# Kernel tuning notes

Hardware: AMD Instinct MI355X
Metric: run time of the kernel (lower is better)

Reference implementation:

```python
import jax, jax.numpy as jnp
import numpy as np

LAYERS = 2
HEADS = 4
TYPE_IDX = 1  # type='logic' -> 1
HIDDEN = 256
HEAD_DIM = HIDDEN // HEADS
EPS = 1e-6


def setup_inputs() -> dict:
    key = jax.random.key(0)
    ks = jax.random.split(key, 12)
    B, S, H = 4, 2048, HIDDEN
    inputs = jax.random.normal(ks[0], (B, S, H), jnp.float32)
    graphs = jax.random.uniform(ks[1], (B, 2, S, S), jnp.float32)
    biases_batch = jax.random.normal(ks[2], (B, 2, S, S), jnp.float32)
    s_h = 1.0 / np.sqrt(H).astype(np.float32)
    s_d = 1.0 / np.sqrt(HEAD_DIM).astype(np.float32)
    gc_w = jax.random.normal(ks[3], (LAYERS, H, H), jnp.float32) * s_h
    gc_b = jnp.zeros((LAYERS, H), jnp.float32)
    attn_w = jax.random.normal(ks[4], (LAYERS, HEAD_DIM, H), jnp.float32) * s_h  # conv1 (1x1) weight
    attn_a = jax.random.normal(ks[5], (LAYERS, HEAD_DIM), jnp.float32) * s_d     # conv2_1 (1x1) weight
    ln_a = jnp.ones((H,), jnp.float32)
    ln_b = jnp.zeros((H,), jnp.float32)
    w1 = jax.random.normal(ks[6], (H, H), jnp.float32) * s_h
    w1b = jnp.zeros((H,), jnp.float32)
    w2 = jax.random.normal(ks[7], (H, H), jnp.float32) * s_h
    w2b = jnp.zeros((H,), jnp.float32)
    return dict(inputs=inputs, graphs=graphs, biases_batch=biases_batch,
                gc_w=gc_w, gc_b=gc_b, attn_w=attn_w, attn_a=attn_a,
                ln_a=ln_a, ln_b=ln_b, w1=w1, w1b=w1b, w2=w2, w2b=w2b)


def reference(inputs, graphs, biases_batch, gc_w, gc_b, attn_w, attn_a, ln_a, ln_b, w1, w1b, w2, w2b):
    adj = graphs[:, TYPE_IDX]          # [b,s,s]
    bias = biases_batch[:, TYPE_IDX]   # [b,s,s]
    x0 = inputs
    x = inputs
    for i in range(LAYERS):
        # GraphConvolution: adj @ (x @ W) + b
        mf = jnp.einsum('bij,bjh->bih', adj, x @ gc_w[i]) + gc_b[i]
        # Node_Attn_head (NOTE: original uses conv2_1 for BOTH f_1 and f_2)
        seq_fts = jnp.einsum('bsh,dh->bsd', mf, attn_w[i])      # [b,s,d]
        f = seq_fts @ attn_a[i]                                  # [b,s]
        logits = jax.nn.leaky_relu(f[:, :, None] + f[:, None, :])  # f_2^T + f_1 -> [b,s,s]
        coefs = jax.nn.softmax(logits + bias, axis=1)            # Softmax(dim=1)
        ret = jax.nn.leaky_relu(jnp.einsum('bij,bjd->bid', coefs, seq_fts))  # [b,s,d]
        # shared attention head across all HEADS -> identical outputs, concatenated
        x = jnp.tile(ret, (1, 1, HEADS)) + x
    # LayerNorm (torch.std is unbiased -> ddof=1), residual to original inputs
    mean = x.mean(-1, keepdims=True)
    std = jnp.std(x, axis=-1, keepdims=True, ddof=1)
    g = ln_a * (x - mean) / (std + EPS) + ln_b + x0
    # PositionwiseFeedForward (dropout inactive in eval)
    ff = jax.nn.relu(g @ w1.T + w1b) @ w2.T + w2b
    return ff + g
```

## Files before the change

### kernel.cpp

```cpp
#include <hip/hip_runtime.h>
#include <math.h>

#define BB 4
#define SS 2048
#define HH 256
#define DD 64
#define NLAYERS 2
#define NPART 128

#define XSC  (1.f/64.f)
#define XSCI 64.f
#define FSC  (1.f/256.f)
#define WSC  256.f
#define LNWSC 5.5451774444795624f
#define EC1  190781.31f
#define CWC  1.3418535e-3f

typedef _Float16 f16;
typedef f16 half8 __attribute__((ext_vector_type(8)));
typedef f16 half4 __attribute__((ext_vector_type(4)));
typedef float f32x4 __attribute__((ext_vector_type(4)));
#define MFMA16(a, b, c) __builtin_amdgcn_mfma_f32_16x16x32_f16(a, b, c, 0, 0, 0)

__device__ __forceinline__ float lrelu(float v) { return v > 0.f ? v : 0.01f * v; }
__device__ __forceinline__ int enc(float f) { int i = __float_as_int(f); return i >= 0 ? i : (i ^ 0x7fffffff); }
__device__ __forceinline__ float dec(int k) { int i = k >= 0 ? k : (k ^ 0x7fffffff); return __int_as_float(i); }
__device__ __forceinline__ void split8(const float* v, half8& h, half8& l) {
    #pragma unroll
    for (int e = 0; e < 8; ++e) {
        f16 hh = (f16)v[e]; h[e] = hh; l[e] = (f16)((v[e] - (float)hh) * 2048.f);
    }
}

__global__ __launch_bounds__(256) void prep_all(
    const float* __restrict__ gc_w, const float* __restrict__ gc_b,
    const float* __restrict__ attn_w,
    f16* __restrict__ WysH, f16* __restrict__ WysL, float* __restrict__ by,
    const float* __restrict__ w1, const float* __restrict__ w2,
    f16* __restrict__ w1h, f16* __restrict__ w1l,
    f16* __restrict__ w2h, f16* __restrict__ w2l, int* __restrict__ FMXi,
    const float* __restrict__ inputs, f16* __restrict__ xh, f16* __restrict__ xl)
{
    if (blockIdx.x >= 128) {
        long i = ((long)(blockIdx.x - 128) * 256 + threadIdx.x) * 8;
        float4 a = *(const float4*)&inputs[i];
        float4 b = *(const float4*)&inputs[i + 4];
        float v[8] = {a.x * XSC, a.y * XSC, a.z * XSC, a.w * XSC,
                      b.x * XSC, b.y * XSC, b.z * XSC, b.w * XSC};
        half8 h, l; split8(v, h, l);
        *(half8*)&xh[i] = h; *(half8*)&xl[i] = l;
        return;
    }
    int L = blockIdx.x >> 6, d = blockIdx.x & 63;
    int h = threadIdx.x;
    const float* gwr = gc_w + (long)L * HH * HH + (long)h * HH;
    const float* aw = attn_w + (long)L * DD * HH + (long)d * HH;
    float acc = 0.f;
    #pragma unroll 4
    for (int hp = 0; hp < HH; hp += 4) {
        float4 g4 = *(const float4*)&gwr[hp];
        float4 a4 = *(const float4*)&aw[hp];
        acc += g4.x * a4.x + g4.y * a4.y + g4.z * a4.z + g4.w * a4.w;
    }
    f16 hh = (f16)acc;
    WysH[((long)L * DD + d) * HH + h] = hh;
    WysL[((long)L * DD + d) * HH + h] = (f16)((acc - (float)hh) * 2048.f);
    if (h == 0) {
        float ba = 0.f;
        const float* gb = gc_b + (long)L * HH;
        for (int hp = 0; hp < HH; ++hp) ba += gb[hp] * aw[hp];
        by[L * DD + d] = ba;
    }
    int gt = blockIdx.x * 256 + h;
    #pragma unroll
    for (int p = 0; p < 4; ++p) {
        int e = gt * 4 + p;
        if (e < 65536) {
            float v = w1[e]; f16 x = (f16)v;
            w1h[e] = x; w1l[e] = (f16)((v - (float)x) * 2048.f);
        } else {
            int e2 = e - 65536;
            float v = w2[e2]; f16 x = (f16)v;
            w2h[e2] = x; w2l[e2] = (f16)((v - (float)x) * 2048.f);
        }
    }
    if (blockIdx.x == 0 && h < 2 * BB) FMXi[h] = enc(-1e30f);
}

__global__ __launch_bounds__(256) void y_mfma(
    const f16* __restrict__ xh, const f16* __restrict__ xl,
    const f16* __restrict__ WyhL, const f16* __restrict__ WylL,
    f16* __restrict__ yTh, f16* __restrict__ yTl)
{
    const int tid = threadIdx.x;
    const int w = tid >> 6, l = tid & 63;
    const int gw = blockIdx.x * 4 + w;
    const int b = gw >> 7, st = gw & 127;
    const int s0 = st * 16;
    const int lr = l & 15, kg = (l >> 4) * 8;
    const f16* Aph = xh + ((long)b * SS + s0 + lr) * HH;
    const f16* Apl = xl + ((long)b * SS + s0 + lr) * HH;
    f32x4 acch[4] = {}, accm[4] = {};
    #pragma unroll
    for (int k0 = 0; k0 < HH; k0 += 32) {
        half8 ah = *(const half8*)(Aph + k0 + kg);
        half8 al = *(const half8*)(Apl + k0 + kg);
        #pragma unroll
        for (int dt = 0; dt < 4; ++dt) {
            long boff = (long)(dt * 16 + lr) * HH + k0 + kg;
            half8 bh = *(const half8*)(WyhL + boff);
            half8 bl = *(const half8*)(WylL + boff);
            acch[dt] = MFMA16(ah, bh, acch[dt]);
            accm[dt] = MFMA16(ah, bl, accm[dt]);
            accm[dt] = MFMA16(al, bh, accm[dt]);
        }
    }
    const int rg0 = (l >> 4) * 4;
    #pragma unroll
    for (int dt = 0; dt < 4; ++dt) {
        int d = dt * 16 + lr;
        half4 h4, l4;
        #pragma unroll
        for (int rr = 0; rr < 4; ++rr) {
            float v = acch[dt][rr] + accm[dt][rr] * (1.f / 2048.f);
            f16 hh = (f16)v; h4[rr] = hh; l4[rr] = (f16)((v - (float)hh) * 2048.f);
        }
        long ob = ((long)b * DD + d) * SS + s0 + rg0;
        *(half4*)(yTh + ob) = h4;
        *(half4*)(yTl + ob) = l4;
    }
}

__global__ __launch_bounds__(512, 2) void ftp_fused(
    const float* __restrict__ adjB,
    const f16* __restrict__ yTh, const f16* __restrict__ yTl,
    const float* __restrict__ byL, const float* __restrict__ aaL,
    float* __restrict__ F, f16* __restrict__ fTh, f16* __restrict__ fTl,
    int* __restrict__ fmxSlot)
{
    __shared__ float Ls[8][16][68];
    __shared__ float fmaxS[16];
    const int b = blockIdx.y;
    const int i0 = blockIdx.x * 16;
    const int tid = threadIdx.x;
    const int w = tid >> 6, l = tid & 63, lr = l & 15, kg = (l >> 4) * 8;
    const float* Arow = adjB + (long)b * 2 * SS * SS + (long)(i0 + lr) * SS;
    const f16* Bh = yTh + ((long)b * DD + lr) * SS;
    const f16* Bl = yTl + ((long)b * DD + lr) * SS;

    f32x4 acch[4] = {}, accm[4] = {};
    #pragma unroll
    for (int ks = 0; ks < 256; ks += 32) {
        int k = w * 256 + ks + kg;
        float4 a0 = *(const float4*)(Arow + k);
        float4 a1 = *(const float4*)(Arow + k + 4);
        float av[8] = {a0.x, a0.y, a0.z, a0.w, a1.x, a1.y, a1.z, a1.w};
        half8 ah, al; split8(av, ah, al);
        #pragma unroll
        for (int dt = 0; dt < 4; ++dt) {
            long off = (long)dt * 16 * SS + k;
            half8 bh = *(const half8*)(Bh + off);
            half8 bl = *(const half8*)(Bl + off);
            acch[dt] = MFMA16(ah, bh, acch[dt]);
            accm[dt] = MFMA16(ah, bl, accm[dt]);
            accm[dt] = MFMA16(al, bh, accm[dt]);
        }
    }
    const int rg0 = (l >> 4) * 4;
    #pragma unroll
    for (int dt = 0; dt < 4; ++dt)
        #pragma unroll
        for (int rr = 0; rr < 4; ++rr)
            Ls[w][rg0 + rr][dt * 16 + lr] = acch[dt][rr] + accm[dt][rr] * (1.f / 2048.f);
    __syncthreads();

    {
        int r = tid >> 5, q = tid & 31, c0 = q * 2;
        float s0 = 0.f, s1 = 0.f;
        #pragma unroll
        for (int ww = 0; ww < 8; ++ww) { s0 += Ls[ww][r][c0]; s1 += Ls[ww][r][c0 + 1]; }
        s0 = s0 * XSCI + byL[c0];
        s1 = s1 * XSCI + byL[c0 + 1];
        Ls[0][r][c0] = s0; Ls[0][r][c0 + 1] = s1;
        float dot = s0 * aaL[c0] + s1 * aaL[c0 + 1];
        dot += __shfl_xor(dot, 1, 64);
        dot += __shfl_xor(dot, 2, 64);
        dot += __shfl_xor(dot, 4, 64);
        dot += __shfl_xor(dot, 8, 64);
        dot += __shfl_xor(dot, 16, 64);
        if (q == 0) { F[b * SS + i0 + r] = dot; fmaxS[r] = dot; }
    }
    __syncthreads();
    if (tid == 0) {
        float m = -1e30f;
        #pragma unroll
        for (int r = 0; r < 16; ++r) m = fmaxf(m, fmaxS[r]);
        atomicMax(fmxSlot + b, enc(m));
    }
    if (tid < 256) {
        int d = tid >> 2, sq = (tid & 3) * 4;
        half4 h4, l4;
        #pragma unroll
        for (int e = 0; e < 4; ++e) {
            float v = Ls[0][sq + e][d] * FSC;
            f16 hh = (f16)v; h4[e] = hh; l4[e] = (f16)((v - (float)hh) * 2048.f);
        }
        long ob = ((long)b * DD + d) * SS + i0 + sq;
        *(half4*)(fTh + ob) = h4;
        *(half4*)(fTl + ob) = l4;
    }
}

__global__ __launch_bounds__(512) void col_stats_part(
    const float* __restrict__ biasb, const float* __restrict__ f,
    const int* __restrict__ fmxSlot,
    float* __restrict__ partS, float* __restrict__ Mv, f16* __restrict__ EhL)
{
    __shared__ float fs[32];
    const int b = blockIdx.z;
    const int chunk = blockIdx.y;
    const int half = threadIdx.x >> 8;
    const int t = threadIdx.x & 255;
    const int j0 = blockIdx.x * 1024 + t * 4;
    const float* bb = biasb + (long)b * 2 * SS * SS;
    const int ibase = chunk * 32 + half * 16;

    if (threadIdx.x < 32) fs[threadIdx.x] = f[b * SS + chunk * 32 + threadIdx.x];

    float fj[4], M[4], s[4] = {0.f, 0.f, 0.f, 0.f};
    const float fmx = dec(fmxSlot[b]);
    #pragma unroll
    for (int q = 0; q < 4; ++q) {
        fj[q] = f[b * SS + j0 + q];
        M[q] = lrelu(fmx + fj[q]) + 8.f;
    }
    __syncthreads();

    #pragma unroll
    for (int ii = 0; ii < 16; ii += 2) {
        float fi0 = fs[half * 16 + ii], fi1 = fs[half * 16 + ii + 1];
        float4 b0 = *(const float4*)&bb[(long)(ibase + ii) * SS + j0];
        float4 b1 = *(const float4*)&bb[(long)(ibase + ii + 1) * SS + j0];
        float e00 = __expf(lrelu(fi0 + fj[0]) + b0.x - M[0]);
        float e01 = __expf(lrelu(fi0 + fj[1]) + b0.y - M[1]);
        float e02 = __expf(lrelu(fi0 + fj[2]) + b0.z - M[2]);
        float e03 = __expf(lrelu(fi0 + fj[3]) + b0.w - M[3]);
        float e10 = __expf(lrelu(fi1 + fj[0]) + b1.x - M[0]);
        float e11 = __expf(lrelu(fi1 + fj[1]) + b1.y - M[1]);
        float e12 = __expf(lrelu(fi1 + fj[2]) + b1.z - M[2]);
        float e13 = __expf(lrelu(fi1 + fj[3]) + b1.w - M[3]);
        s[0] += e00 + e10; s[1] += e01 + e11;
        s[2] += e02 + e12; s[3] += e03 + e13;
        if (EhL) {
            half4 h0, h1;
            h0[0] = (f16)(e00 * EC1); h0[1] = (f16)(e01 * EC1);
            h0[2] = (f16)(e02 * EC1); h0[3] = (f16)(e03 * EC1);
            h1[0] = (f16)(e10 * EC1); h1[1] = (f16)(e11 * EC1);
            h1[2] = (f16)(e12 * EC1); h1[3] = (f16)(e13 * EC1);
            *(half4*)&EhL[((long)b * SS + ibase + ii) * SS + j0] = h0;
            *(half4*)&EhL[((long)b * SS + ibase + ii + 1) * SS + j0] = h1;
        }
    }
    const int c = chunk * 2 + half;
    #pragma unroll
    for (int q = 0; q < 4; ++q)
        partS[((long)c * BB + b) * SS + j0 + q] = s[q];
    if (c == 0) {
        #pragma unroll
        for (int q = 0; q < 4; ++q) Mv[b * SS + j0 + q] = M[q];
    }
}

__global__ __launch_bounds__(256) void col_stats_merge(
    const float* __restrict__ partS, const float* __restrict__ Mv,
    float* __restrict__ Cv, float* __restrict__ Cw)
{
    __shared__ float red[4][64];
    const int b = blockIdx.y;
    const int jl = threadIdx.x & 63;
    const int p = threadIdx.x >> 6;
    const int j = blockIdx.x * 64 + jl;
    float s = 0.f;
    #pragma unroll
    for (int k = 0; k < 32; ++k)
        s += partS[((long)(p * 32 + k) * BB + b) * SS + j];
    red[p][jl] = s;
    __syncthreads();
    if (p == 0) {
        float tot = ((red[0][jl] + red[1][jl]) + (red[2][jl] + red[3][jl]));
        Cv[b * SS + j] = LNWSC - __logf(tot) - Mv[b * SS + j];
        Cw[b * SS + j] = CWC / tot;
    }
}

__global__ __launch_bounds__(512, 2) void pvp_fused(
    const float* __restrict__ biasb, const float* __restrict__ f,
    const float* __restrict__ Cv,
    const f16* __restrict__ fTh, const f16* __restrict__ fTl,
    const float* __restrict__ xin, float* __restrict__ X,
    f16* __restrict__ xh, f16* __restrict__ xl)
{
    __shared__ float Ls[8][16][68];
    const int b = blockIdx.y;
    const int i0 = blockIdx.x * 16;
    const int tid = threadIdx.x;
    const int w = tid >> 6, l = tid & 63, lr = l & 15, kg = (l >> 4) * 8;
    const int irow = i0 + lr;
    const float fi = f[b * SS + irow];
    const float* brow = biasb + (long)b * 2 * SS * SS + (long)irow * SS;
    const float* fb = f + b * SS;
    const float* cb = Cv + b * SS;
    const f16* Bh = fTh + ((long)b * DD + lr) * SS;
    const f16* Bl = fTl + ((long)b * DD + lr) * SS;

    f32x4 acch[4] = {}, accm[4] = {};
    #pragma unroll
    for (int jc = 0; jc < 256; jc += 32) {
        const int jb = w * 256 + jc + kg;
        float4 bs0 = *(const float4*)(brow + jb);
        float4 bs1 = *(const float4*)(brow + jb + 4);
        float4 fj0 = *(const float4*)(fb + jb);
        float4 fj1 = *(const float4*)(fb + jb + 4);
        float4 cj0 = *(const float4*)(cb + jb);
        float4 cj1 = *(const float4*)(cb + jb + 4);
        float wv[8];
        wv[0] = __expf(lrelu(fi + fj0.x) + bs0.x + cj0.x);
        wv[1] = __expf(lrelu(fi + fj0.y) + bs0.y + cj0.y);
        wv[2] = __expf(lrelu(fi + fj0.z) + bs0.z + cj0.z);
        wv[3] = __expf(lrelu(fi + fj0.w) + bs0.w + cj0.w);
        wv[4] = __expf(lrelu(fi + fj1.x) + bs1.x + cj1.x);
        wv[5] = __expf(lrelu(fi + fj1.y) + bs1.y + cj1.y);
        wv[6] = __expf(lrelu(fi + fj1.z) + bs1.z + cj1.z);
        wv[7] = __expf(lrelu(fi + fj1.w) + bs1.w + cj1.w);
        half8 ah, al; split8(wv, ah, al);
        #pragma unroll
        for (int dt = 0; dt < 4; ++dt) {
            long off = (long)dt * 16 * SS + jb;
            half8 bh = *(const half8*)(Bh + off);
            half8 bl = *(const half8*)(Bl + off);
            acch[dt] = MFMA16(ah, bh, acch[dt]);
            accm[dt] = MFMA16(ah, bl, accm[dt]);
            accm[dt] = MFMA16(al, bh, accm[dt]);
        }
    }
    const int rg0 = (l >> 4) * 4;
    #pragma unroll
    for (int dt = 0; dt < 4; ++dt)
        #pragma unroll
        for (int rr = 0; rr < 4; ++rr)
            Ls[w][rg0 + rr][dt * 16 + lr] = acch[dt][rr] + accm[dt][rr] * (1.f / 2048.f);
    __syncthreads();

    {
        int r = tid >> 5, q = tid & 31, dq = q * 2;
        float v0 = 0.f, v1 = 0.f;
        #pragma unroll
        for (int ww = 0; ww < 8; ++ww) { v0 += Ls[ww][r][dq]; v1 += Ls[ww][r][dq + 1]; }
        v0 = lrelu(v0); v1 = lrelu(v1);
        long rowoff = ((long)b * SS + i0 + r) * HH;
        #pragma unroll
        for (int rep = 0; rep < 4; ++rep) {
            long off = rowoff + rep * DD + dq;
            float o0 = v0 + xin[off];
            float o1 = v1 + xin[off + 1];
            X[off] = o0; X[off + 1] = o1;
            float s0 = o0 * XSC, s1 = o1 * XSC;
            f16 h0 = (f16)s0, h1 = (f16)s1;
            xh[off] = h0; xl[off] = (f16)((s0 - (float)h0) * 2048.f);
            xh[off + 1] = h1; xl[off + 1] = (f16)((s1 - (float)h1) * 2048.f);
        }
    }
}

__global__ __launch_bounds__(512, 2) void pvp_fused2(
    const f16* __restrict__ Eh, const float* __restrict__ Cw,
    const f16* __restrict__ fTh, const f16* __restrict__ fTl,
    const float* __restrict__ xin, float* __restrict__ X)
{
    __shared__ float Ls[8][16][68];
    const int b = blockIdx.y;
    const int i0 = blockIdx.x * 16;
    const int tid = threadIdx.x;
    const int w = tid >> 6, l = tid & 63, lr = l & 15, kg = (l >> 4) * 8;
    const int irow = i0 + lr;
    const f16* Erow = Eh + ((long)b * SS + irow) * SS;
    const float* cw = Cw + (long)b * SS;
    const f16* Bh = fTh + ((long)b * DD + lr) * SS;
    const f16* Bl = fTl + ((long)b * DD + lr) * SS;

    f32x4 acch[4] = {}, accm[4] = {};
    #pragma unroll
    for (int jc = 0; jc < 256; jc += 32) {
        const int jb = w * 256 + jc + kg;
        half8 ev = *(const half8*)(Erow + jb);
        float4 c0 = *(const float4*)(cw + jb);
        float4 c1 = *(const float4*)(cw + jb + 4);
        float wv[8];
        wv[0] = (float)ev[0] * c0.x; wv[1] = (float)ev[1] * c0.y;
        wv[2] = (float)ev[2] * c0.z; wv[3] = (float)ev[3] * c0.w;
        wv[4] = (float)ev[4] * c1.x; wv[5] = (float)ev[5] * c1.y;
        wv[6] = (float)ev[6] * c1.z; wv[7] = (float)ev[7] * c1.w;
        half8 ah, al; split8(wv, ah, al);
        #pragma unroll
        for (int dt = 0; dt < 4; ++dt) {
            long off = (long)dt * 16 * SS + jb;
            half8 bh = *(const half8*)(Bh + off);
            half8 bl = *(const half8*)(Bl + off);
            acch[dt] = MFMA16(ah, bh, acch[dt]);
            accm[dt] = MFMA16(ah, bl, accm[dt]);
            accm[dt] = MFMA16(al, bh, accm[dt]);
        }
    }
    const int rg0 = (l >> 4) * 4;
    #pragma unroll
    for (int dt = 0; dt < 4; ++dt)
        #pragma unroll
        for (int rr = 0; rr < 4; ++rr)
            Ls[w][rg0 + rr][dt * 16 + lr] = acch[dt][rr] + accm[dt][rr] * (1.f / 2048.f);
    __syncthreads();

    {
        int r = tid >> 5, q = tid & 31, dq = q * 2;
        float v0 = 0.f, v1 = 0.f;
        #pragma unroll
        for (int ww = 0; ww < 8; ++ww) { v0 += Ls[ww][r][dq]; v1 += Ls[ww][r][dq + 1]; }
        v0 = lrelu(v0); v1 = lrelu(v1);
        long rowoff = ((long)b * SS + i0 + r) * HH;
        #pragma unroll
        for (int rep = 0; rep < 4; ++rep) {
            long off = rowoff + rep * DD + dq;
            X[off] = v0 + xin[off];
            X[off + 1] = v1 + xin[off + 1];
        }
    }
}

__global__ __launch_bounds__(256) void layernorm_g(
    const float* __restrict__ x, const float* __restrict__ x0,
    const float* __restrict__ lna, const float* __restrict__ lnb,
    float* __restrict__ g, f16* __restrict__ gh, f16* __restrict__ gl)
{
    const int wave = threadIdx.x >> 6, lane = threadIdx.x & 63;
    const long row = (long)blockIdx.x * 4 + wave;
    const int c0 = lane * 4;
    float4 v = *(const float4*)&x[row * HH + c0];
    float s = v.x + v.y + v.z + v.w;
    #pragma unroll
    for (int off = 32; off; off >>= 1) s += __shfl_xor(s, off, 64);
    float mean = s * (1.f / HH);
    float dx = v.x - mean, dy = v.y - mean, dz = v.z - mean, dw = v.w - mean;
    float sq = dx * dx + dy * dy + dz * dz + dw * dw;
    #pragma unroll
    for (int off = 32; off; off >>= 1) sq += __shfl_xor(sq, off, 64);
    float stdv = sqrtf(sq * (1.f / (HH - 1)));
    float rinv = 1.f / (stdv + 1e-6f);
    float4 la = *(const float4*)&lna[c0];
    float4 lb = *(const float4*)&lnb[c0];
    float4 xo = *(const float4*)&x0[row * HH + c0];
    float gv[4];
    gv[0] = la.x * dx * rinv + lb.x + xo.x;
    gv[1] = la.y * dy * rinv + lb.y + xo.y;
    gv[2] = la.z * dz * rinv + lb.z + xo.z;
    gv[3] = la.w * dw * rinv + lb.w + xo.w;
    *(float4*)&g[row * HH + c0] = *(float4*)gv;
    half4 h4, l4;
    #pragma unroll
    for (int e = 0; e < 4; ++e) {
        f16 hh = (f16)gv[e]; h4[e] = hh; l4[e] = (f16)((gv[e] - (float)hh) * 2048.f);
    }
    *(half4*)&gh[row * HH + c0] = h4;
    *(half4*)&gl[row * HH + c0] = l4;
}

__global__ __launch_bounds__(256) void ffn_mfma(
    const f16* __restrict__ Ah, const f16* __restrict__ Al,
    const f16* __restrict__ Bh, const f16* __restrict__ Bl,
    const float* __restrict__ bias, const float* __restrict__ res,
    float* __restrict__ outF, f16* __restrict__ outH, f16* __restrict__ outL,
    int doRelu)
{
    __shared__ float Ls[64][68];
    const int i0 = blockIdx.x * 64, j0 = blockIdx.y * 64;
    const int tid = threadIdx.x;
    const int w = tid >> 6, l = tid & 63, lr = l & 15, kg = (l >> 4) * 8;
    const f16* Aph = Ah + ((long)i0 + w * 16 + lr) * HH;
    const f16* Apl = Al + ((long)i0 + w * 16 + lr) * HH;
    f32x4 acch[4] = {}, accm[4] = {};
    #pragma unroll
    for (int k0 = 0; k0 < HH; k0 += 32) {
        half8 ah = *(const half8*)(Aph + k0 + kg);
        half8 al = *(const half8*)(Apl + k0 + kg);
        #pragma unroll
        for (int dt = 0; dt < 4; ++dt) {
            long boff = ((long)(j0 + dt * 16 + lr)) * HH + k0 + kg;
            half8 bh = *(const half8*)(Bh + boff);
            half8 bl = *(const half8*)(Bl + boff);
            acch[dt] = MFMA16(ah, bh, acch[dt]);
            accm[dt] = MFMA16(ah, bl, accm[dt]);
            accm[dt] = MFMA16(al, bh, accm[dt]);
        }
    }
    const int rg0 = (l >> 4) * 4;
    #pragma unroll
    for (int dt = 0; dt < 4; ++dt) {
        float bj = bias[j0 + dt * 16 + lr];
        #pragma unroll
        for (int rr = 0; rr < 4; ++rr) {
            float v = acch[dt][rr] + accm[dt][rr] * (1.f / 2048.f) + bj;
            if (doRelu) v = fmaxf(v, 0.f);
            Ls[w * 16 + rg0 + rr][dt * 16 + lr] = v;
        }
    }
    __syncthreads();
    int s = tid >> 2, nq = (tid & 3) * 16;
    long go = ((long)i0 + s) * HH + j0 + nq;
    if (outF) {
        #pragma unroll
        for (int q = 0; q < 4; ++q) {
            float4 v = *(float4*)&Ls[s][nq + q * 4];
            if (res) {
                float4 r = *(const float4*)&res[go + q * 4];
                v.x += r.x; v.y += r.y; v.z += r.z; v.w += r.w;
            }
            *(float4*)&outF[go + q * 4] = v;
        }
    } else {
        float v0[8], v1[8];
        #pragma unroll
        for (int e = 0; e < 8; ++e) { v0[e] = Ls[s][nq + e]; v1[e] = Ls[s][nq + 8 + e]; }
        half8 h0, l0, h1, l1; split8(v0, h0, l0); split8(v1, h1, l1);
        *(half8*)&outH[go] = h0; *(half8*)&outH[go + 8] = h1;
        *(half8*)&outL[go] = l0; *(half8*)&outL[go + 8] = l1;
    }
}

extern "C" void kernel_launch(void* const* d_in, const int* in_sizes, int n_in,
                              void* d_out, int out_size, void* d_ws, size_t ws_size,
                              hipStream_t stream)
{
    const float* inputs = (const float*)d_in[0];
    const float* graphs = (const float*)d_in[1];
    const float* biases = (const float*)d_in[2];
    const float* gc_w   = (const float*)d_in[3];
    const float* gc_b   = (const float*)d_in[4];
    const float* attn_w = (const float*)d_in[5];
    const float* attn_a = (const float*)d_in[6];
    const float* ln_a   = (const float*)d_in[7];
    const float* ln_b   = (const float*)d_in[8];
    const float* w1     = (const float*)d_in[9];
    const float* w1b    = (const float*)d_in[10];
    const float* w2     = (const float*)d_in[11];
    const float* w2b    = (const float*)d_in[12];
    float* out = (float*)d_out;

    float* ws   = (float*)d_ws;
    float* X    = ws;
    float* G    = ws + 2097152;
    float* PTS  = ws + 4194304;
    float* F    = ws + 5242880;
    float* Mv   = ws + 5251072;
    float* Cv   = ws + 5259264;
    float* Cw   = ws + 5267456;
    float* by   = ws + 5275648;
    int*   FMXi = (int*)(ws + 5275776);
    f16* WysH   = (f16*)(ws + 5275904);
    f16* WysL   = (f16*)(ws + 5292288);
    f16* yTh    = (f16*)(ws + 5308672);
    f16* yTl    = (f16*)(ws + 5570816);
    f16* fTh    = (f16*)(ws + 5832960);
    f16* fTl    = (f16*)(ws + 6095104);
    f16* xh     = (f16*)(ws + 6357248);
    f16* xl     = (f16*)(ws + 7405824);
    f16* gh     = (f16*)(ws + 8454400);
    f16* gl     = (f16*)(ws + 9502976);
    f16* h1h    = (f16*)(ws + 10551552);
    f16* h1l    = (f16*)(ws + 11600128);
    f16* w1h    = (f16*)(ws + 12648704);
    f16* w1l    = (f16*)(ws + 12681472);
    f16* w2h    = (f16*)(ws + 12714240);
    f16* w2l    = (f16*)(ws + 12747008);
    f16* Eh     = (f16*)(ws + 12779776);

    const float* adjBase  = graphs + (long)SS * SS;
    const float* biasBase = biases + (long)SS * SS;

    prep_all<<<1152, 256, 0, stream>>>(gc_w, gc_b, attn_w, WysH, WysL, by,
                                       w1, w2, w1h, w1l, w2h, w2l, FMXi,
                                       inputs, xh, xl);

    for (int L = 0; L < NLAYERS; ++L) {
        y_mfma<<<128, 256, 0, stream>>>(xh, xl,
            WysH + (long)L * DD * HH, WysL + (long)L * DD * HH, yTh, yTl);
        ftp_fused<<<dim3(128, BB), 512, 0, stream>>>(
            adjBase, yTh, yTl, by + L * DD, attn_a + (long)L * DD,
            F, fTh, fTl, FMXi + L * BB);
        col_stats_part<<<dim3(2, 64, BB), 512, 0, stream>>>(
            biasBase, F, FMXi + L * BB, PTS, Mv, (L == 1) ? Eh : (f16*)nullptr);
        col_stats_merge<<<dim3(32, BB), 256, 0, stream>>>(PTS, Mv, Cv, Cw);
        if (L == 0) {
            pvp_fused<<<dim3(128, BB), 512, 0, stream>>>(
                biasBase, F, Cv, fTh, fTl, inputs, X, xh, xl);
        } else {
            pvp_fused2<<<dim3(128, BB), 512, 0, stream>>>(
                Eh, Cw, fTh, fTl, X, X);
        }
    }

    layernorm_g<<<2048, 256, 0, stream>>>(X, inputs, ln_a, ln_b, G, gh, gl);
    ffn_mfma<<<dim3(128, 4), 256, 0, stream>>>(gh, gl, w1h, w1l, w1b,
                                               nullptr, nullptr, h1h, h1l, 1);
    ffn_mfma<<<dim3(128, 4), 256, 0, stream>>>(h1h, h1l, w2h, w2l, w2b,
                                               G, out, nullptr, nullptr, 0);
}
```

Before: 298.6 us.

## Fuse column-stat merge via last-block counter and fold LayerNorm into final PV kernel

Removes the separate col_stats_merge kernel: each col_stats block bumps an atomic counter, and the last block per (batch, column-half) reduces the 128 partial sums and writes Cv/Cw, recomputing M instead of storing Mv. The LayerNorm kernel is also folded into the layer-2 PV kernel, which now computes row mean/std with wave shuffles and writes G and the split-f16 copies directly, skipping the X round-trip. This saves two launches and some global traffic. The cost is that the serial tail reduction now runs in only a few blocks, and the LN writes are scalar and less coalesced.

```diff
diff --git a/kernel.cpp b/kernel.cpp
--- a/kernel.cpp
+++ b/kernel.cpp
@@ -6,7 +6,6 @@
 #define HH 256
 #define DD 64
 #define NLAYERS 2
-#define NPART 128
 
 #define XSC  (1.f/64.f)
 #define XSCI 64.f
@@ -38,7 +37,8 @@
     f16* __restrict__ WysH, f16* __restrict__ WysL, float* __restrict__ by,
     const float* __restrict__ w1, const float* __restrict__ w2,
     f16* __restrict__ w1h, f16* __restrict__ w1l,
-    f16* __restrict__ w2h, f16* __restrict__ w2l, int* __restrict__ FMXi,
+    f16* __restrict__ w2h, f16* __restrict__ w2l,
+    int* __restrict__ FMXi, int* __restrict__ CNTi,
     const float* __restrict__ inputs, f16* __restrict__ xh, f16* __restrict__ xl)
 {
     if (blockIdx.x >= 128) {
@@ -85,6 +85,7 @@
         }
     }
     if (blockIdx.x == 0 && h < 2 * BB) FMXi[h] = enc(-1e30f);
+    if (blockIdx.x == 1 && h < 32) CNTi[h] = 0;
 }
 
 __global__ __launch_bounds__(256) void y_mfma(
@@ -211,12 +212,14 @@
     }
 }
 
-__global__ __launch_bounds__(512) void col_stats_part(
+__global__ __launch_bounds__(512) void col_stats_fused(
     const float* __restrict__ biasb, const float* __restrict__ f,
     const int* __restrict__ fmxSlot,
-    float* __restrict__ partS, float* __restrict__ Mv, f16* __restrict__ EhL)
+    float* __restrict__ partS, f16* __restrict__ EhL,
+    int* __restrict__ cnt, float* __restrict__ Cv, float* __restrict__ Cw)
 {
     __shared__ float fs[32];
+    __shared__ int lastS;
     const int b = blockIdx.z;
     const int chunk = blockIdx.y;
     const int half = threadIdx.x >> 8;
@@ -265,31 +268,28 @@
     #pragma unroll
     for (int q = 0; q < 4; ++q)
         partS[((long)c * BB + b) * SS + j0 + q] = s[q];
-    if (c == 0) {
-        #pragma unroll
-        for (int q = 0; q < 4; ++q) Mv[b * SS + j0 + q] = M[q];
-    }
-}
-
-__global__ __launch_bounds__(256) void col_stats_merge(
-    const float* __restrict__ partS, const float* __restrict__ Mv,
-    float* __restrict__ Cv, float* __restrict__ Cw)
-{
-    __shared__ float red[4][64];
-    const int b = blockIdx.y;
-    const int jl = threadIdx.x & 63;
-    const int p = threadIdx.x >> 6;
-    const int j = blockIdx.x * 64 + jl;
-    float s = 0.f;
-    #pragma unroll
-    for (int k = 0; k < 32; ++k)
-        s += partS[((long)(p * 32 + k) * BB + b) * SS + j];
-    red[p][jl] = s;
-    __syncthreads();
-    if (p == 0) {
-        float tot = ((red[0][jl] + red[1][jl]) + (red[2][jl] + red[3][jl]));
-        Cv[b * SS + j] = LNWSC - __logf(tot) - Mv[b * SS + j];
-        Cw[b * SS + j] = CWC / tot;
+
+    __threadfence();
+    __syncthreads();
+    if (threadIdx.x == 0) {
+        int old = atomicAdd(cnt + b * 2 + blockIdx.x, 1);
+        lastS = (old == 63) ? 1 : 0;
+    }
+    __syncthreads();
+    if (lastS) {
+        int j = blockIdx.x * 1024 + threadIdx.x * 2;
+        float2 tot = {0.f, 0.f};
+        for (int cc = 0; cc < 128; ++cc) {
+            float2 u = *(const float2*)&partS[((long)cc * BB + b) * SS + j];
+            tot.x += u.x; tot.y += u.y;
+        }
+        float fja = f[b * SS + j], fjb = f[b * SS + j + 1];
+        float Ma = lrelu(fmx + fja) + 8.f;
+        float Mb = lrelu(fmx + fjb) + 8.f;
+        Cv[b * SS + j]     = LNWSC - __logf(tot.x) - Ma;
+        Cv[b * SS + j + 1] = LNWSC - __logf(tot.y) - Mb;
+        Cw[b * SS + j]     = CWC / tot.x;
+        Cw[b * SS + j + 1] = CWC / tot.y;
     }
 }
 
@@ -372,10 +372,12 @@
     }
 }
 
-__global__ __launch_bounds__(512, 2) void pvp_fused2(
+__global__ __launch_bounds__(512, 2) void pvp_fused2_ln(
     const f16* __restrict__ Eh, const float* __restrict__ Cw,
     const f16* __restrict__ fTh, const f16* __restrict__ fTl,
-    const float* __restrict__ xin, float* __restrict__ X)
+    const float* __restrict__ xin, const float* __restrict__ x0,
+    const float* __restrict__ lna, const float* __restrict__ lnb,
+    float* __restrict__ G, f16* __restrict__ gh, f16* __restrict__ gl)
 {
     __shared__ float Ls[8][16][68];
     const int b = blockIdx.y;
@@ -426,50 +428,37 @@
         for (int ww = 0; ww < 8; ++ww) { v0 += Ls[ww][r][dq]; v1 += Ls[ww][r][dq + 1]; }
         v0 = lrelu(v0); v1 = lrelu(v1);
         long rowoff = ((long)b * SS + i0 + r) * HH;
+        float o[8];
+        float s = 0.f;
         #pragma unroll
         for (int rep = 0; rep < 4; ++rep) {
             long off = rowoff + rep * DD + dq;
-            X[off] = v0 + xin[off];
-            X[off + 1] = v1 + xin[off + 1];
-        }
-    }
-}
-
-__global__ __launch_bounds__(256) void layernorm_g(
-    const float* __restrict__ x, const float* __restrict__ x0,
-    const float* __restrict__ lna, const float* __restrict__ lnb,
-    float* __restrict__ g, f16* __restrict__ gh, f16* __restrict__ gl)
-{
-    const int wave = threadIdx.x >> 6, lane = threadIdx.x & 63;
-    const long row = (long)blockIdx.x * 4 + wave;
-    const int c0 = lane * 4;
-    float4 v = *(const float4*)&x[row * HH + c0];
-    float s = v.x + v.y + v.z + v.w;
-    #pragma unroll
-    for (int off = 32; off; off >>= 1) s += __shfl_xor(s, off, 64);
-    float mean = s * (1.f / HH);
-    float dx = v.x - mean, dy = v.y - mean, dz = v.z - mean, dw = v.w - mean;
-    float sq = dx * dx + dy * dy + dz * dz + dw * dw;
-    #pragma unroll
-    for (int off = 32; off; off >>= 1) sq += __shfl_xor(sq, off, 64);
-    float stdv = sqrtf(sq * (1.f / (HH - 1)));
-    float rinv = 1.f / (stdv + 1e-6f);
-    float4 la = *(const float4*)&lna[c0];
-    float4 lb = *(const float4*)&lnb[c0];
-    float4 xo = *(const float4*)&x0[row * HH + c0];
-    float gv[4];
-    gv[0] = la.x * dx * rinv + lb.x + xo.x;
-    gv[1] = la.y * dy * rinv + lb.y + xo.y;
-    gv[2] = la.z * dz * rinv + lb.z + xo.z;
-    gv[3] = la.w * dw * rinv + lb.w + xo.w;
-    *(float4*)&g[row * HH + c0] = *(float4*)gv;
-    half4 h4, l4;
-    #pragma unroll
-    for (int e = 0; e < 4; ++e) {
-        f16 hh = (f16)gv[e]; h4[e] = hh; l4[e] = (f16)((gv[e] - (float)hh) * 2048.f);
-    }
-    *(half4*)&gh[row * HH + c0] = h4;
-    *(half4*)&gl[row * HH + c0] = l4;
+            o[2 * rep]     = v0 + xin[off];
+            o[2 * rep + 1] = v1 + xin[off + 1];
+            s += o[2 * rep] + o[2 * rep + 1];
+        }
+        #pragma unroll
+        for (int off = 16; off; off >>= 1) s += __shfl_xor(s, off, 64);
+        float mean = s * (1.f / HH);
+        float sq = 0.f;
+        #pragma unroll
+        for (int e = 0; e < 8; ++e) { float d = o[e] - mean; sq += d * d; }
+        #pragma unroll
+        for (int off = 16; off; off >>= 1) sq += __shfl_xor(sq, off, 64);
+        float stdv = sqrtf(sq * (1.f / (HH - 1)));
+        float rinv = 1.f / (stdv + 1e-6f);
+        #pragma unroll
+        for (int rep = 0; rep < 4; ++rep) {
+            int col = rep * DD + dq;
+            long off = rowoff + col;
+            float g0 = lna[col] * (o[2 * rep] - mean) * rinv + lnb[col] + x0[off];
+            float g1 = lna[col + 1] * (o[2 * rep + 1] - mean) * rinv + lnb[col + 1] + x0[off + 1];
+            G[off] = g0; G[off + 1] = g1;
+            f16 h0 = (f16)g0, h1 = (f16)g1;
+            gh[off] = h0; gl[off] = (f16)((g0 - (float)h0) * 2048.f);
+            gh[off + 1] = h1; gl[off + 1] = (f16)((g1 - (float)h1) * 2048.f);
+        }
+    }
 }
 
 __global__ __launch_bounds__(256) void ffn_mfma(
@@ -558,34 +547,34 @@
     float* G    = ws + 2097152;
     float* PTS  = ws + 4194304;
     float* F    = ws + 5242880;
-    float* Mv   = ws + 5251072;
-    float* Cv   = ws + 5259264;
-    float* Cw   = ws + 5267456;
-    float* by   = ws + 5275648;
-    int*   FMXi = (int*)(ws + 5275776);
-    f16* WysH   = (f16*)(ws + 5275904);
-    f16* WysL   = (f16*)(ws + 5292288);
-    f16* yTh    = (f16*)(ws + 5308672);
-    f16* yTl    = (f16*)(ws + 5570816);
-    f16* fTh    = (f16*)(ws + 5832960);
-    f16* fTl    = (f16*)(ws + 6095104);
-    f16* xh     = (f16*)(ws + 6357248);
-    f16* xl     = (f16*)(ws + 7405824);
-    f16* gh     = (f16*)(ws + 8454400);
-    f16* gl     = (f16*)(ws + 9502976);
-    f16* h1h    = (f16*)(ws + 10551552);
-    f16* h1l    = (f16*)(ws + 11600128);
-    f16* w1h    = (f16*)(ws + 12648704);
-    f16* w1l    = (f16*)(ws + 12681472);
-    f16* w2h    = (f16*)(ws + 12714240);
-    f16* w2l    = (f16*)(ws + 12747008);
-    f16* Eh     = (f16*)(ws + 12779776);
+    float* Cv   = ws + 5251072;
+    float* Cw   = ws + 5259264;
+    float* by   = ws + 5267456;
+    int*   FMXi = (int*)(ws + 5267584);
+    int*   CNTi = (int*)(ws + 5267712);
+    f16* WysH   = (f16*)(ws + 5267840);
+    f16* WysL   = (f16*)(ws + 5284224);
+    f16* yTh    = (f16*)(ws + 5300608);
+    f16* yTl    = (f16*)(ws + 5562752);
+    f16* fTh    = (f16*)(ws + 5824896);
+    f16* fTl    = (f16*)(ws + 6087040);
+    f16* xh     = (f16*)(ws + 6349184);
+    f16* xl     = (f16*)(ws + 7397760);
+    f16* gh     = (f16*)(ws + 8446336);
+    f16* gl     = (f16*)(ws + 9494912);
+    f16* h1h    = (f16*)(ws + 10543488);
+    f16* h1l    = (f16*)(ws + 11592064);
+    f16* w1h    = (f16*)(ws + 12640640);
+    f16* w1l    = (f16*)(ws + 12673408);
+    f16* w2h    = (f16*)(ws + 12706176);
+    f16* w2l    = (f16*)(ws + 12738944);
+    f16* Eh     = (f16*)(ws + 12771712);
 
     const float* adjBase  = graphs + (long)SS * SS;
     const float* biasBase = biases + (long)SS * SS;
 
     prep_all<<<1152, 256, 0, stream>>>(gc_w, gc_b, attn_w, WysH, WysL, by,
-                                       w1, w2, w1h, w1l, w2h, w2l, FMXi,
+                                       w1, w2, w1h, w1l, w2h, w2l, FMXi, CNTi,
                                        inputs, xh, xl);
 
     for (int L = 0; L < NLAYERS; ++L) {
@@ -594,19 +583,18 @@
         ftp_fused<<<dim3(128, BB), 512, 0, stream>>>(
             adjBase, yTh, yTl, by + L * DD, attn_a + (long)L * DD,
             F, fTh, fTl, FMXi + L * BB);
-        col_stats_part<<<dim3(2, 64, BB), 512, 0, stream>>>(
-            biasBase, F, FMXi + L * BB, PTS, Mv, (L == 1) ? Eh : (f16*)nullptr);
-        col_stats_merge<<<dim3(32, BB), 256, 0, stream>>>(PTS, Mv, Cv, Cw);
+        col_stats_fused<<<dim3(2, 64, BB), 512, 0, stream>>>(
+            biasBase, F, FMXi + L * BB, PTS,
+            (L == 1) ? Eh : (f16*)nullptr, CNTi + L * 8, Cv, Cw);
         if (L == 0) {
             pvp_fused<<<dim3(128, BB), 512, 0, stream>>>(
                 biasBase, F, Cv, fTh, fTl, inputs, X, xh, xl);
         } else {
-            pvp_fused2<<<dim3(128, BB), 512, 0, stream>>>(
-                Eh, Cw, fTh, fTl, X, X);
-        }
-    }
-
-    layernorm_g<<<2048, 256, 0, stream>>>(X, inputs, ln_a, ln_b, G, gh, gl);
+            pvp_fused2_ln<<<dim3(128, BB), 512, 0, stream>>>(
+                Eh, Cw, fTh, fTl, X, inputs, ln_a, ln_b, G, gh, gl);
+        }
+    }
+
     ffn_mfma<<<dim3(128, 4), 256, 0, stream>>>(gh, gl, w1h, w1l, w1b,
                                                nullptr, nullptr, h1h, h1l, 1);
     ffn_mfma<<<dim3(128, 4), 256, 0, stream>>>(h1h, h1l, w2h, w2l, w2b,
```

Result: slower. 509.9 us (median of 3 runs) (+70.8%).
